# Kernel optimization log

Measured on AMD Instinct MI355X. Metric: run time of the kernel, lower is better.

Reference implementation:

```python
import jax, jax.numpy as jnp
import numpy as np

GROUPS = 32
HEADS = 8
EPS = 1e-5

def setup_inputs() -> dict:
    key = jax.random.key(0)
    ks = jax.random.split(key, 5)
    C = 512
    x = jax.random.normal(ks[0], (8, C, 32, 32), dtype=jnp.float32)
    gn_w = jnp.ones((C,), dtype=jnp.float32)
    gn_b = jnp.zeros((C,), dtype=jnp.float32)
    qkv_w = jax.random.normal(ks[1], (3 * C, C), dtype=jnp.float32) * 0.02
    qkv_b = jnp.zeros((3 * C,), dtype=jnp.float32)
    proj_w = jax.random.normal(ks[2], (C, C), dtype=jnp.float32) * 0.02
    proj_b = jnp.zeros((C,), dtype=jnp.float32)
    return {"x": x, "gn_w": gn_w, "gn_b": gn_b, "qkv_w": qkv_w,
            "qkv_b": qkv_b, "proj_w": proj_w, "proj_b": proj_b}

def reference(x, gn_w, gn_b, qkv_w, qkv_b, proj_w, proj_b):
    B, C, H, W = x.shape
    d = C // HEADS
    # GroupNorm(32, C)
    xg = x.reshape(B, GROUPS, C // GROUPS, H, W)
    mean = xg.mean(axis=(2, 3, 4), keepdims=True)
    var = xg.var(axis=(2, 3, 4), keepdims=True)
    h = ((xg - mean) * jax.lax.rsqrt(var + EPS)).reshape(B, C, H, W)
    h = h * gn_w[None, :, None, None] + gn_b[None, :, None, None]
    # 1x1 conv QKV == channel matmul
    qkv = jnp.einsum('bchw,oc->bohw', h, qkv_w) + qkv_b[None, :, None, None]
    qkv = qkv.reshape(B, 3, HEADS, d, H * W)
    q, k, v = qkv[:, 0], qkv[:, 1], qkv[:, 2]  # [B, heads, d, HW]
    scale = d ** (-0.5)
    # weight[b,h,q,k] = sum_d q[b,h,d,q] * k[b,h,d,k] * scale
    attn = jax.nn.softmax(jnp.einsum('bhdq,bhdk->bhqk', q, k) * scale, axis=-1)
    # out[b,h,d,q] = sum_k v[b,h,d,k] * attn[b,h,q,k]
    out = jnp.einsum('bhdk,bhqk->bhdq', v, attn).reshape(B, C, H, W)
    out = jnp.einsum('bchw,oc->bohw', out, proj_w) + proj_b[None, :, None, None]
    return out + x
```

## Files before the change

kernel.cpp:

```cpp
#include <hip/hip_runtime.h>
#include <math.h>

#define B_    8
#define C_    512
#define HW_   1024
#define O3_   1536
#define HEADS_ 8
#define D_    64
#define G_    32
#define CPG_  16
#define EPS_  1e-5f
#define M_TOT 8192

#define QSCALE (0.125f * 1.44269504088896f)

typedef __bf16 bf16x8 __attribute__((ext_vector_type(8)));
typedef __bf16 bf16x4 __attribute__((ext_vector_type(4)));
typedef float  f32x4  __attribute__((ext_vector_type(4)));

__device__ __forceinline__ void async_copy16(void* lds, const void* g) {
  __builtin_amdgcn_global_load_lds(
      (const __attribute__((address_space(1))) unsigned int*)g,
      (__attribute__((address_space(3))) unsigned int*)lds, 16, 0, 0);
}

__global__ __launch_bounds__(256) void k_gn(const float* __restrict__ x,
                                            const float* __restrict__ gw,
                                            const float* __restrict__ gb,
                                            __bf16* __restrict__ h,
                                            const float* __restrict__ qw,
                                            const float* __restrict__ pw,
                                            __bf16* __restrict__ qwb,
                                            __bf16* __restrict__ pwb) {
  __shared__ float red[10];
  __shared__ __bf16 T[16 * 1032];
  if (blockIdx.x >= B_ * G_) {
    int i = (blockIdx.x - B_ * G_) * 256 + threadIdx.x;
    if (i < O3_ * C_ / 4) {
      float4 v = ((const float4*)qw)[i];
      bf16x4 o = {(__bf16)v.x, (__bf16)v.y, (__bf16)v.z, (__bf16)v.w};
      ((bf16x4*)qwb)[i] = o;
    }
    if (i < C_ * C_ / 4) {
      float4 v = ((const float4*)pw)[i];
      bf16x4 o = {(__bf16)v.x, (__bf16)v.y, (__bf16)v.z, (__bf16)v.w};
      ((bf16x4*)pwb)[i] = o;
    }
    return;
  }
  int bg = blockIdx.x;
  int b = bg >> 5, g = bg & 31;
  const float* xg = x + ((size_t)(b * C_) + g * CPG_) * HW_;
  const float4* xg4 = (const float4*)xg;
  int tid = threadIdx.x;

  float s = 0.f, ss = 0.f;
  for (int i = tid; i < CPG_ * HW_ / 4; i += 256) {
    float4 v = xg4[i];
    s += v.x + v.y + v.z + v.w;
    ss += v.x * v.x + v.y * v.y + v.z * v.z + v.w * v.w;
  }
  for (int off = 32; off > 0; off >>= 1) {
    s  += __shfl_down(s, off, 64);
    ss += __shfl_down(ss, off, 64);
  }
  int wv = tid >> 6;
  if ((tid & 63) == 0) { red[wv] = s; red[4 + wv] = ss; }
  __syncthreads();
  if (tid == 0) {
    float S  = red[0] + red[1] + red[2] + red[3];
    float SS = red[4] + red[5] + red[6] + red[7];
    float mean = S / (float)(CPG_ * HW_);
    float var  = SS / (float)(CPG_ * HW_) - mean * mean;
    red[8] = mean;
    red[9] = rsqrtf(var + EPS_);
  }
  __syncthreads();
  float mean = red[8], rstd = red[9];

  for (int i = tid; i < CPG_ * HW_ / 4; i += 256) {
    int c = i >> 8;
    int hw4 = (i & 255) * 4;
    float ga = gw[g * CPG_ + c], be = gb[g * CPG_ + c];
    float4 v = xg4[i];
    bf16x4 pk;
    pk[0] = (__bf16)((v.x - mean) * rstd * ga + be);
    pk[1] = (__bf16)((v.y - mean) * rstd * ga + be);
    pk[2] = (__bf16)((v.z - mean) * rstd * ga + be);
    pk[3] = (__bf16)((v.w - mean) * rstd * ga + be);
    *(bf16x4*)(&T[c * 1032 + hw4]) = pk;
  }
  __syncthreads();

  __bf16* hb = h + (size_t)b * HW_ * C_ + g * CPG_;
  for (int j = tid; j < 2 * HW_; j += 256) {
    int hw = j >> 1, c8 = (j & 1) * 8;
    bf16x8 v;
#pragma unroll
    for (int jj = 0; jj < 8; jj++) v[jj] = T[(c8 + jj) * 1032 + hw];
    *(bf16x8*)(hb + (size_t)hw * C_ + c8) = v;
  }
}

#define BK 64
__device__ __forceinline__ void gemm128_core(const __bf16* __restrict__ aBase,
                                             const __bf16* __restrict__ bBase,
                                             __bf16* As, __bf16* Bs,
                                             f32x4 acc[4][4]) {
  int t = threadIdx.x;
  int lane = t & 63;
  int l16 = lane & 15, quad = lane >> 4;
  int wv = t >> 6;
  int wm = (wv >> 1) * 64, wn = (wv & 1) * 64;

  int rsub = lane >> 3;
  int chunk = (lane & 7) ^ rsub;
  const __bf16* ag = aBase + (size_t)(wv * 32 + rsub) * C_ + chunk * 8;
  const __bf16* bg = bBase + (size_t)(wv * 32 + rsub) * C_ + chunk * 8;
  __bf16* la = As + wv * 2048 + lane * 8;
  __bf16* lb = Bs + wv * 2048 + lane * 8;
  int sw = l16 & 7;

  for (int k0 = 0; k0 < C_; k0 += BK) {
#pragma unroll
    for (int s = 0; s < 4; s++) {
      async_copy16(la + s * 512, ag + (size_t)(s * 8) * C_ + k0);
      async_copy16(lb + s * 512, bg + (size_t)(s * 8) * C_ + k0);
    }
    __syncthreads();
#pragma unroll
    for (int h = 0; h < 2; h++) {
      bf16x8 af[4], bf[4];
#pragma unroll
      for (int i = 0; i < 4; i++) {
        af[i] = *(const bf16x8*)(As + (wm + i * 16 + l16) * BK +
                                 ((h * 4 + quad) ^ sw) * 8);
        bf[i] = *(const bf16x8*)(Bs + (wn + i * 16 + l16) * BK +
                                 ((h * 4 + quad) ^ sw) * 8);
      }
#pragma unroll
      for (int i = 0; i < 4; i++)
#pragma unroll
        for (int j = 0; j < 4; j++)
          acc[i][j] = __builtin_amdgcn_mfma_f32_16x16x32_bf16(af[i], bf[j],
                                                              acc[i][j], 0, 0, 0);
    }
    __syncthreads();
  }
}

__global__ __launch_bounds__(256) void k_qkv(const __bf16* __restrict__ h,
                                             const __bf16* __restrict__ w,
                                             const float* __restrict__ bias,
                                             __bf16* __restrict__ y,
                                             __bf16* __restrict__ vT) {
  __shared__ __align__(16) __bf16 As[128 * BK];
  __shared__ __align__(16) __bf16 Bs[128 * BK];
  int m0 = blockIdx.x * 128, n0 = blockIdx.y * 128;
  f32x4 acc[4][4];
#pragma unroll
  for (int i = 0; i < 4; i++)
#pragma unroll
    for (int j = 0; j < 4; j++) acc[i][j] = f32x4{0.f, 0.f, 0.f, 0.f};
  gemm128_core(h + (size_t)m0 * C_, w + (size_t)n0 * C_, As, Bs, acc);

  int lane = threadIdx.x & 63, wv = threadIdx.x >> 6;
  int l16 = lane & 15, quad = lane >> 4;
  int wm = (wv >> 1) * 64, wn = (wv & 1) * 64;

  if (n0 >= 2 * C_) {
    int bb = m0 >> 10;
    int tokBase = (m0 & 1023) + wm + quad * 4;
#pragma unroll
    for (int j = 0; j < 4; j++) {
      int n = n0 + wn + j * 16 + l16;
      int c = n - 2 * C_;
      float bv = bias[n];
      __bf16* vrow = vT + ((size_t)(bb * C_) + c) * HW_;
#pragma unroll
      for (int i = 0; i < 4; i++) {
        bf16x4 pk;
#pragma unroll
        for (int r = 0; r < 4; r++) pk[r] = (__bf16)(acc[i][j][r] + bv);
        *(bf16x4*)(vrow + tokBase + i * 16) = pk;
      }
    }
  } else {
    float sc = (n0 < C_) ? QSCALE : 1.0f;
#pragma unroll
    for (int j = 0; j < 4; j++) {
      int n = n0 + wn + j * 16 + l16;
      float bv = bias[n];
#pragma unroll
      for (int i = 0; i < 4; i++)
#pragma unroll
        for (int r = 0; r < 4; r++) {
          int m = m0 + wm + i * 16 + quad * 4 + r;
          y[(size_t)m * O3_ + n] = (__bf16)((acc[i][j][r] + bv) * sc);
        }
    }
  }
}

__global__ __launch_bounds__(256) void k_attn(const __bf16* __restrict__ y,
                                              const __bf16* __restrict__ vT,
                                              __bf16* __restrict__ ao) {
  __shared__ __align__(16) __bf16 Ks[2][128 * 64];
  __shared__ __align__(16) __bf16 Vt[2][64 * 128];
  __shared__ __align__(16) __bf16 Pp[4][32 * 36];
  int hd = blockIdx.x, b = blockIdx.y, qt = blockIdx.z;
  int t = threadIdx.x;
  int wv = t >> 6, lane = t & 63, l16 = lane & 15, quad = lane >> 4;
  int q0 = qt * 128 + wv * 32;

  const __bf16* base = y + (size_t)(b * HW_) * O3_ + hd * D_;
  const __bf16* kg = base + C_;
  const __bf16* vtg = vT + ((size_t)(b * C_) + hd * D_) * HW_;

  bf16x8 qb[2][2];
#pragma unroll
  for (int qg = 0; qg < 2; qg++)
#pragma unroll
    for (int dh = 0; dh < 2; dh++)
      qb[qg][dh] = *(const bf16x8*)(base + (size_t)(q0 + qg * 16 + l16) * O3_ +
                                    dh * 32 + quad * 8);

  int kRowSub = lane >> 3;
  int kChunk = (lane & 7) ^ (kRowSub & 7);

  auto stage = [&](int kt, int bi) {
#pragma unroll
    for (int s = 0; s < 4; s++) {
      int row = wv * 32 + s * 8 + kRowSub;
      async_copy16(&Ks[bi][(wv * 32 + s * 8) * 64 + lane * 8],
                   kg + (size_t)(kt + row) * O3_ + kChunk * 8);
    }
#pragma unroll
    for (int s = 0; s < 4; s++) {
      int row = wv * 16 + s * 4 + (lane >> 4);
      int c2 = (lane & 15) ^ (row & 15);
      async_copy16(&Vt[bi][(wv * 16 + s * 4) * 128 + lane * 8],
                   vtg + (size_t)row * HW_ + kt + c2 * 8);
    }
  };

  float l_run[2] = {0.f, 0.f};
  f32x4 o_acc[4][2];
#pragma unroll
  for (int dt = 0; dt < 4; dt++)
#pragma unroll
    for (int qg = 0; qg < 2; qg++) o_acc[dt][qg] = f32x4{0.f, 0.f, 0.f, 0.f};

  stage(0, 0);

  for (int step = 0; step < 8; step++) {
    int bi = step & 1;
    asm volatile("s_waitcnt vmcnt(0)\n\ts_barrier" ::: "memory");
    if (step < 7) stage((step + 1) * 128, bi ^ 1);

    const __bf16* ks = Ks[bi];
    const __bf16* vs = Vt[bi];
#pragma unroll
    for (int kh = 0; kh < 4; kh++) {
      f32x4 st[2][2];
#pragma unroll
      for (int tti = 0; tti < 2; tti++) {
        int row = (kh * 2 + tti) * 16 + l16;
        bf16x8 ka0 = *(const bf16x8*)(&ks[row * 64 + ((quad) ^ (l16 & 7)) * 8]);
        bf16x8 ka1 = *(const bf16x8*)(&ks[row * 64 + ((4 + quad) ^ (l16 & 7)) * 8]);
        f32x4 z = {0.f, 0.f, 0.f, 0.f};
        st[tti][0] = __builtin_amdgcn_mfma_f32_16x16x32_bf16(ka0, qb[0][0], z, 0, 0, 0);
        st[tti][0] = __builtin_amdgcn_mfma_f32_16x16x32_bf16(ka1, qb[0][1], st[tti][0], 0, 0, 0);
        st[tti][1] = __builtin_amdgcn_mfma_f32_16x16x32_bf16(ka0, qb[1][0], z, 0, 0, 0);
        st[tti][1] = __builtin_amdgcn_mfma_f32_16x16x32_bf16(ka1, qb[1][1], st[tti][1], 0, 0, 0);
      }
#pragma unroll
      for (int qg = 0; qg < 2; qg++) {
        float rs = 0.f;
#pragma unroll
        for (int tti = 0; tti < 2; tti++)
#pragma unroll
          for (int r = 0; r < 4; r++) {
            float e = __builtin_amdgcn_exp2f(st[tti][qg][r]);
            st[tti][qg][r] = e;
            rs += e;
          }
        l_run[qg] += rs;
      }
#pragma unroll
      for (int qg = 0; qg < 2; qg++)
#pragma unroll
        for (int tti = 0; tti < 2; tti++) {
          bf16x4 pk;
#pragma unroll
          for (int r = 0; r < 4; r++) pk[r] = (__bf16)st[tti][qg][r];
          *(bf16x4*)(&Pp[wv][(qg * 16 + l16) * 36 + tti * 16 + quad * 4]) = pk;
        }
      asm volatile("s_waitcnt lgkmcnt(0)" ::: "memory");
      bf16x8 pb0 = *(const bf16x8*)(&Pp[wv][l16 * 36 + quad * 8]);
      bf16x8 pb1 = *(const bf16x8*)(&Pp[wv][(16 + l16) * 36 + quad * 8]);
#pragma unroll
      for (int dt = 0; dt < 4; dt++) {
        int vpos = ((kh * 4 + quad) ^ l16) * 8;
        bf16x8 va = *(const bf16x8*)(&vs[(dt * 16 + l16) * 128 + vpos]);
        o_acc[dt][0] = __builtin_amdgcn_mfma_f32_16x16x32_bf16(va, pb0, o_acc[dt][0], 0, 0, 0);
        o_acc[dt][1] = __builtin_amdgcn_mfma_f32_16x16x32_bf16(va, pb1, o_acc[dt][1], 0, 0, 0);
      }
    }
  }

#pragma unroll
  for (int qg = 0; qg < 2; qg++) {
    l_run[qg] += __shfl_xor(l_run[qg], 16, 64);
    l_run[qg] += __shfl_xor(l_run[qg], 32, 64);
  }
  float inv0 = 1.f / l_run[0], inv1 = 1.f / l_run[1];

#pragma unroll
  for (int dt = 0; dt < 4; dt++) {
    bf16x4 p0, p1;
#pragma unroll
    for (int r = 0; r < 4; r++) {
      p0[r] = (__bf16)(o_acc[dt][0][r] * inv0);
      p1[r] = (__bf16)(o_acc[dt][1][r] * inv1);
    }
    int ch = hd * D_ + dt * 16 + quad * 4;
    *(bf16x4*)(ao + (size_t)(b * HW_ + q0 + l16) * C_ + ch) = p0;
    *(bf16x4*)(ao + (size_t)(b * HW_ + q0 + 16 + l16) * C_ + ch) = p1;
  }
}

__global__ __launch_bounds__(256) void k_proj(const __bf16* __restrict__ ao,
                                              const __bf16* __restrict__ w,
                                              const float* __restrict__ bias,
                                              const float* __restrict__ x,
                                              float* __restrict__ out) {
  __shared__ __align__(16) __bf16 As[128 * BK];
  __shared__ __align__(16) __bf16 Bs[64 * BK];
  int n0 = blockIdx.x * 64, m0 = blockIdx.y * 128;
  int t = threadIdx.x;
  int lane = t & 63, l16 = lane & 15, quad = lane >> 4;
  int wv = t >> 6;
  int wm = (wv >> 1) * 64, wn = (wv & 1) * 32;

  int rsub = lane >> 3;
  int chunk = (lane & 7) ^ rsub;
  const __bf16* ag = w + (size_t)(m0 + wv * 32 + rsub) * C_ + chunk * 8;
  const __bf16* bg = ao + (size_t)(n0 + wv * 16 + rsub) * C_ + chunk * 8;
  __bf16* la = As + wv * 2048 + lane * 8;
  __bf16* lb = Bs + wv * 1024 + lane * 8;
  int sw = l16 & 7;

  f32x4 acc[4][2];
#pragma unroll
  for (int i = 0; i < 4; i++)
#pragma unroll
    for (int j = 0; j < 2; j++) acc[i][j] = f32x4{0.f, 0.f, 0.f, 0.f};

  for (int k0 = 0; k0 < C_; k0 += BK) {
#pragma unroll
    for (int s = 0; s < 4; s++)
      async_copy16(la + s * 512, ag + (size_t)(s * 8) * C_ + k0);
#pragma unroll
    for (int s = 0; s < 2; s++)
      async_copy16(lb + s * 512, bg + (size_t)(s * 8) * C_ + k0);
    __syncthreads();
#pragma unroll
    for (int h = 0; h < 2; h++) {
      bf16x8 af[4], bf[2];
#pragma unroll
      for (int i = 0; i < 4; i++)
        af[i] = *(const bf16x8*)(As + (wm + i * 16 + l16) * BK +
                                 ((h * 4 + quad) ^ sw) * 8);
#pragma unroll
      for (int j = 0; j < 2; j++)
        bf[j] = *(const bf16x8*)(Bs + (wn + j * 16 + l16) * BK +
                                 ((h * 4 + quad) ^ sw) * 8);
#pragma unroll
      for (int i = 0; i < 4; i++)
#pragma unroll
        for (int j = 0; j < 2; j++)
          acc[i][j] = __builtin_amdgcn_mfma_f32_16x16x32_bf16(af[i], bf[j],
                                                              acc[i][j], 0, 0, 0);
    }
    __syncthreads();
  }

  int bb = n0 >> 10;
#pragma unroll
  for (int i = 0; i < 4; i++)
#pragma unroll
    for (int r = 0; r < 4; r++) {
      int o = m0 + wm + i * 16 + quad * 4 + r;
      float bv = bias[o];
#pragma unroll
      for (int j = 0; j < 2; j++) {
        int n = n0 + wn + j * 16 + l16;
        int hw = n & 1023;
        size_t idx = ((size_t)(bb * C_ + o)) * HW_ + hw;
        out[idx] = acc[i][j][r] + bv + x[idx];
      }
    }
}

extern "C" void kernel_launch(void* const* d_in, const int* in_sizes, int n_in,
                              void* d_out, int out_size, void* d_ws, size_t ws_size,
                              hipStream_t stream) {
  const float* x      = (const float*)d_in[0];
  const float* gn_w   = (const float*)d_in[1];
  const float* gn_b   = (const float*)d_in[2];
  const float* qkv_w  = (const float*)d_in[3];
  const float* qkv_b  = (const float*)d_in[4];
  const float* proj_w = (const float*)d_in[5];
  const float* proj_b = (const float*)d_in[6];
  float* out = (float*)d_out;

  char* ws = (char*)d_ws;
  __bf16* h   = (__bf16*)(ws);
  __bf16* qwb = (__bf16*)(ws + 8388608);
  __bf16* pwb = (__bf16*)(ws + 8388608 + 1572864);
  __bf16* yq  = (__bf16*)(ws + 8388608 + 1572864 + 524288);
  __bf16* ao  = (__bf16*)(ws + 8388608 + 1572864 + 524288 + 25165824);
  __bf16* vT  = (__bf16*)(ws + 8388608 + 1572864 + 524288 + 25165824 + 8388608);

  int cvtBlocks = (O3_ * C_ / 4 + 255) / 256;
  k_gn  <<<B_ * G_ + cvtBlocks, 256, 0, stream>>>(x, gn_w, gn_b, h,
                                                  qkv_w, proj_w, qwb, pwb);
  k_qkv <<<dim3(M_TOT / 128, O3_ / 128, 1), 256, 0, stream>>>(h, qwb, qkv_b, yq, vT);
  k_attn<<<dim3(HEADS_, B_, 8), 256, 0, stream>>>(yq, vT, ao);
  k_proj<<<dim3(M_TOT / 64, C_ / 128, 1), 256, 0, stream>>>(ao, pwb, proj_b, x, out);
  (void)in_sizes; (void)n_in; (void)out_size; (void)ws_size;
}
```

Before: 154.9 us.

## Double-buffer LDS in QKV/proj GEMMs and cache GroupNorm input in LDS

The QKV and projection GEMM loops now use two LDS buffers, prefetching the next K tile with async global-to-LDS copies while MFMAs run on the current one, with one waitcnt+barrier per iteration instead of two syncthreads. The GroupNorm kernel stages its 64KB slice of x in LDS so the normalize pass skips the second global read. The weight conversion now uses 256 grid-stride blocks. The extra LDS (64KB in k_gn, doubled tiles in the GEMMs) can lower occupancy, and the prefetch issued right after the barrier shares vmcnt with the wait.

```diff
diff --git a/kernel.cpp b/kernel.cpp
--- a/kernel.cpp
+++ b/kernel.cpp
@@ -33,15 +33,17 @@
                                             __bf16* __restrict__ qwb,
                                             __bf16* __restrict__ pwb) {
   __shared__ float red[10];
+  __shared__ float X[16 * 1024];
   __shared__ __bf16 T[16 * 1032];
   if (blockIdx.x >= B_ * G_) {
-    int i = (blockIdx.x - B_ * G_) * 256 + threadIdx.x;
-    if (i < O3_ * C_ / 4) {
+    int nconv = 256;
+    int i0 = (blockIdx.x - B_ * G_) * 256 + threadIdx.x;
+    for (int i = i0; i < O3_ * C_ / 4; i += nconv * 256) {
       float4 v = ((const float4*)qw)[i];
       bf16x4 o = {(__bf16)v.x, (__bf16)v.y, (__bf16)v.z, (__bf16)v.w};
       ((bf16x4*)qwb)[i] = o;
     }
-    if (i < C_ * C_ / 4) {
+    for (int i = i0; i < C_ * C_ / 4; i += nconv * 256) {
       float4 v = ((const float4*)pw)[i];
       bf16x4 o = {(__bf16)v.x, (__bf16)v.y, (__bf16)v.z, (__bf16)v.w};
       ((bf16x4*)pwb)[i] = o;
@@ -50,13 +52,13 @@
   }
   int bg = blockIdx.x;
   int b = bg >> 5, g = bg & 31;
-  const float* xg = x + ((size_t)(b * C_) + g * CPG_) * HW_;
-  const float4* xg4 = (const float4*)xg;
+  const float4* xg4 = (const float4*)(x + ((size_t)(b * C_) + g * CPG_) * HW_);
   int tid = threadIdx.x;
 
   float s = 0.f, ss = 0.f;
   for (int i = tid; i < CPG_ * HW_ / 4; i += 256) {
     float4 v = xg4[i];
+    ((float4*)X)[i] = v;
     s += v.x + v.y + v.z + v.w;
     ss += v.x * v.x + v.y * v.y + v.z * v.z + v.w * v.w;
   }
@@ -82,7 +84,7 @@
     int c = i >> 8;
     int hw4 = (i & 255) * 4;
     float ga = gw[g * CPG_ + c], be = gb[g * CPG_ + c];
-    float4 v = xg4[i];
+    float4 v = ((const float4*)X)[i];
     bf16x4 pk;
     pk[0] = (__bf16)((v.x - mean) * rstd * ga + be);
     pk[1] = (__bf16)((v.y - mean) * rstd * ga + be);
@@ -103,70 +105,66 @@
 }
 
 #define BK 64
-__device__ __forceinline__ void gemm128_core(const __bf16* __restrict__ aBase,
-                                             const __bf16* __restrict__ bBase,
-                                             __bf16* As, __bf16* Bs,
-                                             f32x4 acc[4][4]) {
-  int t = threadIdx.x;
-  int lane = t & 63;
-  int l16 = lane & 15, quad = lane >> 4;
-  int wv = t >> 6;
-  int wm = (wv >> 1) * 64, wn = (wv & 1) * 64;
-
-  int rsub = lane >> 3;
-  int chunk = (lane & 7) ^ rsub;
-  const __bf16* ag = aBase + (size_t)(wv * 32 + rsub) * C_ + chunk * 8;
-  const __bf16* bg = bBase + (size_t)(wv * 32 + rsub) * C_ + chunk * 8;
-  __bf16* la = As + wv * 2048 + lane * 8;
-  __bf16* lb = Bs + wv * 2048 + lane * 8;
-  int sw = l16 & 7;
-
-  for (int k0 = 0; k0 < C_; k0 += BK) {
-#pragma unroll
-    for (int s = 0; s < 4; s++) {
-      async_copy16(la + s * 512, ag + (size_t)(s * 8) * C_ + k0);
-      async_copy16(lb + s * 512, bg + (size_t)(s * 8) * C_ + k0);
-    }
-    __syncthreads();
-#pragma unroll
-    for (int h = 0; h < 2; h++) {
-      bf16x8 af[4], bf[4];
-#pragma unroll
-      for (int i = 0; i < 4; i++) {
-        af[i] = *(const bf16x8*)(As + (wm + i * 16 + l16) * BK +
-                                 ((h * 4 + quad) ^ sw) * 8);
-        bf[i] = *(const bf16x8*)(Bs + (wn + i * 16 + l16) * BK +
-                                 ((h * 4 + quad) ^ sw) * 8);
-      }
-#pragma unroll
-      for (int i = 0; i < 4; i++)
-#pragma unroll
-        for (int j = 0; j < 4; j++)
-          acc[i][j] = __builtin_amdgcn_mfma_f32_16x16x32_bf16(af[i], bf[j],
-                                                              acc[i][j], 0, 0, 0);
-    }
-    __syncthreads();
-  }
-}
-
 __global__ __launch_bounds__(256) void k_qkv(const __bf16* __restrict__ h,
                                              const __bf16* __restrict__ w,
                                              const float* __restrict__ bias,
                                              __bf16* __restrict__ y,
                                              __bf16* __restrict__ vT) {
-  __shared__ __align__(16) __bf16 As[128 * BK];
-  __shared__ __align__(16) __bf16 Bs[128 * BK];
+  __shared__ __align__(16) __bf16 As[2][128 * BK];
+  __shared__ __align__(16) __bf16 Bs[2][128 * BK];
   int m0 = blockIdx.x * 128, n0 = blockIdx.y * 128;
+  int t = threadIdx.x;
+  int lane = t & 63, l16 = lane & 15, quad = lane >> 4;
+  int wv = t >> 6;
+  int wm = (wv >> 1) * 64, wn = (wv & 1) * 64;
+
+  int rsub = lane >> 3;
+  int chunk = (lane & 7) ^ rsub;
+  const __bf16* ag = h + (size_t)(m0 + wv * 32 + rsub) * C_ + chunk * 8;
+  const __bf16* bg = w + (size_t)(n0 + wv * 32 + rsub) * C_ + chunk * 8;
+  int sw = l16 & 7;
+
+  auto stage = [&](int k0, int bi) {
+    __bf16* la = As[bi] + wv * 2048 + lane * 8;
+    __bf16* lb = Bs[bi] + wv * 2048 + lane * 8;
+#pragma unroll
+    for (int s = 0; s < 4; s++) {
+      async_copy16(la + s * 512, ag + (size_t)(s * 8) * C_ + k0);
+      async_copy16(lb + s * 512, bg + (size_t)(s * 8) * C_ + k0);
+    }
+  };
+
   f32x4 acc[4][4];
 #pragma unroll
   for (int i = 0; i < 4; i++)
 #pragma unroll
     for (int j = 0; j < 4; j++) acc[i][j] = f32x4{0.f, 0.f, 0.f, 0.f};
-  gemm128_core(h + (size_t)m0 * C_, w + (size_t)n0 * C_, As, Bs, acc);
-
-  int lane = threadIdx.x & 63, wv = threadIdx.x >> 6;
-  int l16 = lane & 15, quad = lane >> 4;
-  int wm = (wv >> 1) * 64, wn = (wv & 1) * 64;
+
+  stage(0, 0);
+  for (int kk = 0; kk < 8; kk++) {
+    int bi = kk & 1;
+    asm volatile("s_waitcnt vmcnt(0)\n\ts_barrier" ::: "memory");
+    if (kk < 7) stage((kk + 1) * BK, bi ^ 1);
+    const __bf16* as = As[bi];
+    const __bf16* bs = Bs[bi];
+#pragma unroll
+    for (int hh = 0; hh < 2; hh++) {
+      bf16x8 af[4], bf[4];
+#pragma unroll
+      for (int i = 0; i < 4; i++) {
+        af[i] = *(const bf16x8*)(as + (wm + i * 16 + l16) * BK +
+                                 ((hh * 4 + quad) ^ sw) * 8);
+        bf[i] = *(const bf16x8*)(bs + (wn + i * 16 + l16) * BK +
+                                 ((hh * 4 + quad) ^ sw) * 8);
+      }
+#pragma unroll
+      for (int i = 0; i < 4; i++)
+#pragma unroll
+        for (int j = 0; j < 4; j++)
+          acc[i][j] = __builtin_amdgcn_mfma_f32_16x16x32_bf16(af[i], bf[j],
+                                                              acc[i][j], 0, 0, 0);
+    }
+  }
 
   if (n0 >= 2 * C_) {
     int bb = m0 >> 10;
@@ -335,8 +333,8 @@
                                               const float* __restrict__ bias,
                                               const float* __restrict__ x,
                                               float* __restrict__ out) {
-  __shared__ __align__(16) __bf16 As[128 * BK];
-  __shared__ __align__(16) __bf16 Bs[64 * BK];
+  __shared__ __align__(16) __bf16 As[2][128 * BK];
+  __shared__ __align__(16) __bf16 Bs[2][64 * BK];
   int n0 = blockIdx.x * 64, m0 = blockIdx.y * 128;
   int t = threadIdx.x;
   int lane = t & 63, l16 = lane & 15, quad = lane >> 4;
@@ -347,35 +345,43 @@
   int chunk = (lane & 7) ^ rsub;
   const __bf16* ag = w + (size_t)(m0 + wv * 32 + rsub) * C_ + chunk * 8;
   const __bf16* bg = ao + (size_t)(n0 + wv * 16 + rsub) * C_ + chunk * 8;
-  __bf16* la = As + wv * 2048 + lane * 8;
-  __bf16* lb = Bs + wv * 1024 + lane * 8;
   int sw = l16 & 7;
 
-  f32x4 acc[4][2];
-#pragma unroll
-  for (int i = 0; i < 4; i++)
-#pragma unroll
-    for (int j = 0; j < 2; j++) acc[i][j] = f32x4{0.f, 0.f, 0.f, 0.f};
-
-  for (int k0 = 0; k0 < C_; k0 += BK) {
+  auto stage = [&](int k0, int bi) {
+    __bf16* la = As[bi] + wv * 2048 + lane * 8;
+    __bf16* lb = Bs[bi] + wv * 1024 + lane * 8;
 #pragma unroll
     for (int s = 0; s < 4; s++)
       async_copy16(la + s * 512, ag + (size_t)(s * 8) * C_ + k0);
 #pragma unroll
     for (int s = 0; s < 2; s++)
       async_copy16(lb + s * 512, bg + (size_t)(s * 8) * C_ + k0);
-    __syncthreads();
-#pragma unroll
-    for (int h = 0; h < 2; h++) {
+  };
+
+  f32x4 acc[4][2];
+#pragma unroll
+  for (int i = 0; i < 4; i++)
+#pragma unroll
+    for (int j = 0; j < 2; j++) acc[i][j] = f32x4{0.f, 0.f, 0.f, 0.f};
+
+  stage(0, 0);
+  for (int kk = 0; kk < 8; kk++) {
+    int bi = kk & 1;
+    asm volatile("s_waitcnt vmcnt(0)\n\ts_barrier" ::: "memory");
+    if (kk < 7) stage((kk + 1) * BK, bi ^ 1);
+    const __bf16* as = As[bi];
+    const __bf16* bs = Bs[bi];
+#pragma unroll
+    for (int hh = 0; hh < 2; hh++) {
       bf16x8 af[4], bf[2];
 #pragma unroll
       for (int i = 0; i < 4; i++)
-        af[i] = *(const bf16x8*)(As + (wm + i * 16 + l16) * BK +
-                                 ((h * 4 + quad) ^ sw) * 8);
+        af[i] = *(const bf16x8*)(as + (wm + i * 16 + l16) * BK +
+                                 ((hh * 4 + quad) ^ sw) * 8);
 #pragma unroll
       for (int j = 0; j < 2; j++)
-        bf[j] = *(const bf16x8*)(Bs + (wn + j * 16 + l16) * BK +
-                                 ((h * 4 + quad) ^ sw) * 8);
+        bf[j] = *(const bf16x8*)(bs + (wn + j * 16 + l16) * BK +
+                                 ((hh * 4 + quad) ^ sw) * 8);
 #pragma unroll
       for (int i = 0; i < 4; i++)
 #pragma unroll
@@ -383,7 +389,6 @@
           acc[i][j] = __builtin_amdgcn_mfma_f32_16x16x32_bf16(af[i], bf[j],
                                                               acc[i][j], 0, 0, 0);
     }
-    __syncthreads();
   }
 
   int bb = n0 >> 10;
@@ -423,9 +428,8 @@
   __bf16* ao  = (__bf16*)(ws + 8388608 + 1572864 + 524288 + 25165824);
   __bf16* vT  = (__bf16*)(ws + 8388608 + 1572864 + 524288 + 25165824 + 8388608);
 
-  int cvtBlocks = (O3_ * C_ / 4 + 255) / 256;
-  k_gn  <<<B_ * G_ + cvtBlocks, 256, 0, stream>>>(x, gn_w, gn_b, h,
-                                                  qkv_w, proj_w, qwb, pwb);
+  k_gn  <<<B_ * G_ + 256, 256, 0, stream>>>(x, gn_w, gn_b, h,
+                                            qkv_w, proj_w, qwb, pwb);
   k_qkv <<<dim3(M_TOT / 128, O3_ / 128, 1), 256, 0, stream>>>(h, qwb, qkv_b, yq, vT);
   k_attn<<<dim3(HEADS_, B_, 8), 256, 0, stream>>>(yq, vT, ao);
   k_proj<<<dim3(M_TOT / 64, C_ / 128, 1), 256, 0, stream>>>(ao, pwb, proj_b, x, out);
```

Measured after the change: 154.0 us. About the same (-0.6%).
